# Optimization experiments

Measured on AMD Instinct MI355X. Metric: run time of the kernel, lower is better.

Reference implementation:

```python
import jax, jax.numpy as jnp
import numpy as np

N, P, C = 100000, 48, 8
D, H = 64, 4
DH = D // H
FLAG = 7
EPS = 1e-5


def _layer_norm(x, g, b):
    mu = x.mean(-1, keepdims=True)
    var = ((x - mu) ** 2).mean(-1, keepdims=True)
    return (x - mu) * jax.lax.rsqrt(var + EPS) * g + b


def setup_inputs() -> dict:
    key = jax.random.key(0)
    ks = jax.random.split(key, 24)
    w = lambda k, shp: (jax.random.normal(k, shp, dtype=jnp.float32) * 0.05)
    inp = {
        "voxel_features": jax.random.normal(ks[0], (N, D), dtype=jnp.float32),
        "voxels": jax.random.normal(ks[1], (N, P, C), dtype=jnp.float32),
        "pp_w1": w(ks[2], (D, C)), "pp_b1": w(ks[3], (D,)),
        "pp_w2": w(ks[4], (D, D)), "pp_b2": w(ks[5], (D,)),
        "in_proj_w": w(ks[6], (3 * D, D)), "in_proj_b": w(ks[7], (3 * D,)),
        "out_w": w(ks[8], (D, D)), "out_b": w(ks[9], (D,)),
        "ln1_g": jnp.ones((D,), jnp.float32), "ln1_b": jnp.zeros((D,), jnp.float32),
        "ffn_w1": w(ks[10], (2 * D, D)), "ffn_b1": w(ks[11], (2 * D,)),
        "ffn_w2": w(ks[12], (D, 2 * D)), "ffn_b2": w(ks[13], (D,)),
        "ln2_g": jnp.ones((D,), jnp.float32), "ln2_b": jnp.zeros((D,), jnp.float32),
        "op_w1": w(ks[14], (D, D)), "op_b1": w(ks[15], (D,)),
        "op_w2": w(ks[16], (D, D)), "op_b2": w(ks[17], (D,)),
        "num_points": jax.random.randint(ks[18], (N,), 0, P, dtype=jnp.int32),
    }
    return inp


def reference(voxel_features, voxels, pp_w1, pp_b1, pp_w2, pp_b2,
              in_proj_w, in_proj_b, out_w, out_b, ln1_g, ln1_b,
              ffn_w1, ffn_b1, ffn_w2, ffn_b2, ln2_g, ln2_b,
              op_w1, op_b1, op_w2, op_b2, num_points):
    n, p, _ = voxels.shape
    point_mask = jnp.arange(p)[None, :] < num_points[:, None]          # [N,P]
    current_mask = (voxels[:, :, FLAG] > 0.5) & point_mask             # [N,P]
    history_mask = point_mask & ~current_mask                          # [N,P]
    history_present = history_mask.any(axis=1, keepdims=True)          # [N,1]

    point_features = voxels[:, :, :C]

    def masked_mean(vals, mask):
        m = mask.astype(vals.dtype)[..., None]
        counts = jnp.clip(mask.sum(1, keepdims=True), 1, None).astype(vals.dtype)
        return (vals * m).sum(1) / counts                              # [N,C]

    cur_sum = masked_mean(point_features, current_mask)
    his_sum = masked_mean(point_features, history_mask)

    def point_proj(x):
        return jax.nn.relu(x @ pp_w1.T + pp_b1) @ pp_w2.T + pp_b2

    tokens = jnp.stack([voxel_features, point_proj(cur_sum), point_proj(his_sum)], axis=1)  # [N,3,D]

    key_pad = jnp.stack([jnp.zeros((n,), bool),
                         ~current_mask.any(1),
                         ~history_present[:, 0]], axis=1)              # [N,3]

    # multi-head self-attention over 3 tokens
    qkv = tokens @ in_proj_w.T + in_proj_b                             # [N,3,3D]
    q, k, v = jnp.split(qkv, 3, axis=-1)
    q = q.reshape(n, 3, H, DH).transpose(0, 2, 1, 3)                   # [N,H,3,DH]
    k = k.reshape(n, 3, H, DH).transpose(0, 2, 1, 3)
    v = v.reshape(n, 3, H, DH).transpose(0, 2, 1, 3)
    scores = jnp.einsum('nhqd,nhkd->nhqk', q, k) / np.sqrt(DH)
    scores = jnp.where(key_pad[:, None, None, :], -jnp.inf, scores)
    attn = jax.nn.softmax(scores, axis=-1)
    ctx = jnp.einsum('nhqk,nhkd->nhqd', attn, v)                       # [N,H,3,DH]
    ctx = ctx.transpose(0, 2, 1, 3).reshape(n, 3, D)
    attn_out = ctx @ out_w.T + out_b

    tokens = _layer_norm(tokens + attn_out, ln1_g, ln1_b)
    ffn = jax.nn.relu(tokens @ ffn_w1.T + ffn_b1) @ ffn_w2.T + ffn_b2
    tokens = _layer_norm(tokens + ffn, ln2_g, ln2_b)

    refined = jax.nn.relu(tokens[:, 0] @ op_w1.T + op_b1) @ op_w2.T + op_b2
    refined = refined * history_present.astype(refined.dtype)
    return voxel_features + refined
```

## Files before the change

kernel.cpp:

```cpp
#include <hip/hip_runtime.h>


using bf16x8 = __attribute__((ext_vector_type(8))) __bf16;
using f32x4  = __attribute__((ext_vector_type(4))) float;

#define DEV static __device__ __forceinline__
#define SYNC() __syncthreads()

DEV float bf2f(unsigned short u){
  union { unsigned int i; float f; } v; v.i = ((unsigned int)u) << 16; return v.f;
}
DEV unsigned short f2bf(float f){
  union { float f; unsigned int i; } v; v.f = f;
  unsigned int x = v.i;
  x += 0x7FFFu + ((x >> 16) & 1u);
  return (unsigned short)(x >> 16);
}

DEV unsigned short* lp(unsigned short* base, int row, int col){
  int byte = (col << 1) ^ ((row & 7) << 4);
  return (unsigned short*)((char*)base + (row << 7) + byte);
}

DEV bf16x8 ldA(const unsigned short* base, int mt, int kt, int lane){
  int row = mt*16 + (lane & 15);
  int col = kt*32 + ((lane >> 4) << 3);
  return *(const bf16x8*)lp((unsigned short*)base, row, col);
}
DEV bf16x8 ldB(const unsigned short* w, int frag, int lane){
  return *(const bf16x8*)(w + (size_t)frag*512 + (size_t)lane*8);
}
DEV void stC(unsigned short* base, int mt, int nt, f32x4 c, int lane){
  int col  = nt*16 + (lane & 15);
  int row0 = mt*16 + ((lane >> 4) << 2);
  #pragma unroll
  for (int r = 0; r < 4; ++r) *lp(base, row0 + r, col) = f2bf(c[r]);
}
DEV f32x4 MF(bf16x8 a, bf16x8 b, f32x4 c){
  return __builtin_amdgcn_mfma_f32_16x16x32_bf16(a, b, c, 0, 0, 0);
}

DEV void ld16(const unsigned short* base, int row, int col0, float* o){
  uint4 a = *(const uint4*)lp((unsigned short*)base, row, col0);
  uint4 b = *(const uint4*)lp((unsigned short*)base, row, col0 + 8);
  unsigned int w[8] = {a.x, a.y, a.z, a.w, b.x, b.y, b.z, b.w};
  #pragma unroll
  for (int i = 0; i < 8; ++i){
    union { unsigned int u; float f; } lo, hi;
    lo.u = w[i] << 16; hi.u = w[i] & 0xFFFF0000u;
    o[2*i] = lo.f; o[2*i+1] = hi.f;
  }
}
DEV void st16(unsigned short* base, int row, int col0, const float* f){
  unsigned int w[8];
  #pragma unroll
  for (int i = 0; i < 8; ++i)
    w[i] = (unsigned int)f2bf(f[2*i]) | ((unsigned int)f2bf(f[2*i+1]) << 16);
  *(uint4*)lp(base, row, col0)     = make_uint4(w[0], w[1], w[2], w[3]);
  *(uint4*)lp(base, row, col0 + 8) = make_uint4(w[4], w[5], w[6], w[7]);
}

DEV void layer_norm16(f32x4 x[4], const float* g, const float* b, int lane){
  float s[4], s2[4];
  #pragma unroll
  for (int r = 0; r < 4; ++r){
    s[r]  = x[0][r] + x[1][r] + x[2][r] + x[3][r];
    s2[r] = x[0][r]*x[0][r] + x[1][r]*x[1][r] + x[2][r]*x[2][r] + x[3][r]*x[3][r];
  }
  #pragma unroll
  for (int o = 1; o <= 8; o <<= 1){
    #pragma unroll
    for (int r = 0; r < 4; ++r){
      s[r]  += __shfl_xor(s[r],  o);
      s2[r] += __shfl_xor(s2[r], o);
    }
  }
  float mu[4], rs[4];
  #pragma unroll
  for (int r = 0; r < 4; ++r){
    mu[r] = s[r] * (1.f/64.f);
    float var = s2[r] * (1.f/64.f) - mu[r]*mu[r];
    rs[r] = rsqrtf(var + 1e-5f);
  }
  const int cl = lane & 15;
  #pragma unroll
  for (int nt = 0; nt < 4; ++nt){
    float gg = g[nt*16 + cl], bb = b[nt*16 + cl];
    #pragma unroll
    for (int r = 0; r < 4; ++r)
      x[nt][r] = (x[nt][r] - mu[r]) * rs[r] * gg + bb;
  }
}

__global__ void tva_pack_weights(const float* __restrict__ pp_w1, const float* __restrict__ pp_w2,
                                 const float* __restrict__ in_proj_w, const float* __restrict__ out_w,
                                 const float* __restrict__ ffn_w1, const float* __restrict__ ffn_w2,
                                 const float* __restrict__ op_w1, const float* __restrict__ op_w2,
                                 unsigned short* __restrict__ ws)
{
  int b = blockIdx.x, lane = threadIdx.x;
  const float* W; int base, ktiles, K;
  if      (b < 4)  { W = pp_w1;     base = 0;  ktiles = 1; K = 8;   }
  else if (b < 12) { W = pp_w2;     base = 4;  ktiles = 2; K = 64;  }
  else if (b < 36) { W = in_proj_w; base = 12; ktiles = 2; K = 64;  }
  else if (b < 44) { W = out_w;     base = 36; ktiles = 2; K = 64;  }
  else if (b < 60) { W = ffn_w1;    base = 44; ktiles = 2; K = 64;  }
  else if (b < 76) { W = ffn_w2;    base = 60; ktiles = 4; K = 128; }
  else if (b < 84) { W = op_w1;     base = 76; ktiles = 2; K = 64;  }
  else             { W = op_w2;     base = 84; ktiles = 2; K = 64;  }
  int local = b - base;
  int nt = local / ktiles, kt = local % ktiles;
  int n  = nt*16 + (lane & 15);
  int k0 = kt*32 + ((lane >> 4) << 3);
  unsigned short* dst = ws + (size_t)b*512 + (size_t)lane*8;
  #pragma unroll
  for (int i = 0; i < 8; ++i){
    int k = k0 + i;
    float v = (k < K) ? W[(size_t)n*K + k] : 0.0f;
    dst[i] = f2bf(v);
  }
}

__global__ __launch_bounds__(64, 2)
void tva_main(const float* __restrict__ vf, const float* __restrict__ vox,
              const int* __restrict__ num_points,
              const float* __restrict__ pp_b1, const float* __restrict__ pp_b2,
              const float* __restrict__ ipb,  const float* __restrict__ outb,
              const float* __restrict__ ln1g, const float* __restrict__ ln1b,
              const float* __restrict__ f1b,  const float* __restrict__ f2bv,
              const float* __restrict__ ln2g, const float* __restrict__ ln2b,
              const float* __restrict__ o1b,  const float* __restrict__ o2b,
              const unsigned short* __restrict__ wfrag,
              float* __restrict__ out)
{
  __shared__ unsigned short smem[(48 + 48 + 48 + 16) * 64];
  unsigned short* TOK = smem;
  unsigned short* KB  = smem + 48*64;
  unsigned short* VB  = smem + 96*64;
  unsigned short* SB  = smem + 144*64;

  const int lane = threadIdx.x;
  const int v0   = blockIdx.x * 16;
  const int cl   = lane & 15;

  const int vi = lane >> 2, pq = lane & 3;
  const int np = num_points[v0 + vi];
  float cs[8] = {0,0,0,0,0,0,0,0}, hs[8] = {0,0,0,0,0,0,0,0};
  float cc = 0.f, hc = 0.f;
  const float4* vp = (const float4*)(vox + (size_t)(v0 + vi) * 384);
  #pragma unroll
  for (int k = 0; k < 12; ++k){
    int p = pq + (k << 2);
    float4 a = vp[p*2], b = vp[p*2 + 1];
    float pm = (p < np) ? 1.f : 0.f;
    float cm = (b.w > 0.5f) ? pm : 0.f;
    float hm = pm - cm;
    cc += cm; hc += hm;
    cs[0] += a.x*cm; cs[1] += a.y*cm; cs[2] += a.z*cm; cs[3] += a.w*cm;
    cs[4] += b.x*cm; cs[5] += b.y*cm; cs[6] += b.z*cm; cs[7] += b.w*cm;
    hs[0] += a.x*hm; hs[1] += a.y*hm; hs[2] += a.z*hm; hs[3] += a.w*hm;
    hs[4] += b.x*hm; hs[5] += b.y*hm; hs[6] += b.z*hm; hs[7] += b.w*hm;
  }
  #pragma unroll
  for (int o = 1; o <= 2; o <<= 1){
    cc += __shfl_xor(cc, o); hc += __shfl_xor(hc, o);
    #pragma unroll
    for (int j = 0; j < 8; ++j){
      cs[j] += __shfl_xor(cs[j], o);
      hs[j] += __shfl_xor(hs[j], o);
    }
  }
  const float icc = 1.f / fmaxf(cc, 1.f);
  const float ihc = 1.f / fmaxf(hc, 1.f);
  const unsigned int myfw = (cc > 0.f ? 1u : 0u) | (hc > 0.f ? 2u : 0u);

  *lp(KB, vi,      pq*2)     = f2bf(cs[pq*2]   * icc);
  *lp(KB, vi,      pq*2 + 1) = f2bf(cs[pq*2+1] * icc);
  *lp(KB, 16 + vi, pq*2)     = f2bf(hs[pq*2]   * ihc);
  *lp(KB, 16 + vi, pq*2 + 1) = f2bf(hs[pq*2+1] * ihc);
  #pragma unroll
  for (int z = 0; z < 6; ++z){
    *lp(KB, vi,      8 + pq*6 + z) = 0;
    *lp(KB, 16 + vi, 8 + pq*6 + z) = 0;
  }
  SYNC();

  {
    bf16x8 ac  = ldA(KB, 0, 0, lane);
    bf16x8 ahs = ldA(KB, 1, 0, lane);
    #pragma unroll
    for (int nt = 0; nt < 4; ++nt){
      float bb = pp_b1[nt*16 + cl];
      f32x4 c0 = {bb, bb, bb, bb}, c1 = {bb, bb, bb, bb};
      bf16x8 B = ldB(wfrag, 0 + nt, lane);
      c0 = MF(ac,  B, c0);
      c1 = MF(ahs, B, c1);
      #pragma unroll
      for (int r = 0; r < 4; ++r){ c0[r] = fmaxf(c0[r], 0.f); c1[r] = fmaxf(c1[r], 0.f); }
      stC(VB, 0, nt, c0, lane);
      stC(VB, 1, nt, c1, lane);
    }
  }
  SYNC();
  {
    bf16x8 ah[2][2];
    #pragma unroll
    for (int m = 0; m < 2; ++m)
      #pragma unroll
      for (int kt = 0; kt < 2; ++kt) ah[m][kt] = ldA(VB, m, kt, lane);
    #pragma unroll
    for (int m = 0; m < 2; ++m){
      #pragma unroll
      for (int nt = 0; nt < 4; ++nt){
        float bb = pp_b2[nt*16 + cl];
        f32x4 c = {bb, bb, bb, bb};
        c = MF(ah[m][0], ldB(wfrag, 4 + nt*2 + 0, lane), c);
        c = MF(ah[m][1], ldB(wfrag, 4 + nt*2 + 1, lane), c);
        stC(TOK, m + 1, nt, c, lane);
      }
    }
  }
  {
    int rr = lane >> 2, q4 = lane & 3;
    const float* s = vf + (size_t)(v0 + rr)*64 + q4*16;
    float4 x0 = *(const float4*)(s +  0);
    float4 x1 = *(const float4*)(s +  4);
    float4 x2 = *(const float4*)(s +  8);
    float4 x3 = *(const float4*)(s + 12);
    float f[16] = {x0.x,x0.y,x0.z,x0.w, x1.x,x1.y,x1.z,x1.w,
                   x2.x,x2.y,x2.z,x2.w, x3.x,x3.y,x3.z,x3.w};
    st16(TOK, rr, q4*16, f);
  }
  SYNC();

  {
    bf16x8 at[3][2];
    #pragma unroll
    for (int m = 0; m < 3; ++m)
      #pragma unroll
      for (int kt = 0; kt < 2; ++kt) at[m][kt] = ldA(TOK, m, kt, lane);
    #pragma unroll
    for (int nt = 0; nt < 4; ++nt){
      float bb = ipb[nt*16 + cl];
      f32x4 c = {bb, bb, bb, bb};
      c = MF(at[0][0], ldB(wfrag, 12 + nt*2 + 0, lane), c);
      c = MF(at[0][1], ldB(wfrag, 12 + nt*2 + 1, lane), c);
      #pragma unroll
      for (int r = 0; r < 4; ++r) c[r] *= 0.25f;
      stC(SB, 0, nt, c, lane);
    }
    #pragma unroll
    for (int m = 0; m < 3; ++m){
      #pragma unroll
      for (int nt = 0; nt < 4; ++nt){
        int ntg = 4 + nt;
        float bb = ipb[64 + nt*16 + cl];
        f32x4 c = {bb, bb, bb, bb};
        c = MF(at[m][0], ldB(wfrag, 12 + ntg*2 + 0, lane), c);
        c = MF(at[m][1], ldB(wfrag, 12 + ntg*2 + 1, lane), c);
        stC(KB, m, nt, c, lane);
      }
    }
    #pragma unroll
    for (int m = 0; m < 3; ++m){
      #pragma unroll
      for (int nt = 0; nt < 4; ++nt){
        int ntg = 8 + nt;
        float bb = ipb[128 + nt*16 + cl];
        f32x4 c = {bb, bb, bb, bb};
        c = MF(at[m][0], ldB(wfrag, 12 + ntg*2 + 0, lane), c);
        c = MF(at[m][1], ldB(wfrag, 12 + ntg*2 + 1, lane), c);
        stC(VB, m, nt, c, lane);
      }
    }
  }
  SYNC();

  {
    const int av = lane & 15, hh = lane >> 4;
    unsigned int fw = (unsigned int)__shfl((int)myfw, av*4);
    bool ca = (fw & 1u) != 0, hp = (fw & 2u) != 0;
    float q[16]; ld16(SB, av, hh*16, q);
    float sc0, sc1, sc2;
    {
      float kv[16]; float d;
      ld16(KB, av,      hh*16, kv); d = 0.f;
      #pragma unroll
      for (int j = 0; j < 16; ++j) d += q[j]*kv[j];
      sc0 = d;
      ld16(KB, 16 + av, hh*16, kv); d = 0.f;
      #pragma unroll
      for (int j = 0; j < 16; ++j) d += q[j]*kv[j];
      sc1 = d;
      ld16(KB, 32 + av, hh*16, kv); d = 0.f;
      #pragma unroll
      for (int j = 0; j < 16; ++j) d += q[j]*kv[j];
      sc2 = d;
    }
    float m = sc0;
    m = ca ? fmaxf(m, sc1) : m;
    m = hp ? fmaxf(m, sc2) : m;
    float p0 = __expf(sc0 - m);
    float p1 = ca ? __expf(sc1 - m) : 0.f;
    float p2 = hp ? __expf(sc2 - m) : 0.f;
    float inv = 1.f / (p0 + p1 + p2);
    p0 *= inv; p1 *= inv; p2 *= inv;
    float ctx[16];
    {
      float vv[16];
      ld16(VB, av,      hh*16, vv);
      #pragma unroll
      for (int j = 0; j < 16; ++j) ctx[j] = p0*vv[j];
      ld16(VB, 16 + av, hh*16, vv);
      #pragma unroll
      for (int j = 0; j < 16; ++j) ctx[j] += p1*vv[j];
      ld16(VB, 32 + av, hh*16, vv);
      #pragma unroll
      for (int j = 0; j < 16; ++j) ctx[j] += p2*vv[j];
    }
    SYNC();
    st16(SB, av, hh*16, ctx);
  }
  SYNC();

  f32x4 res1[4];
  {
    bf16x8 a0 = ldA(SB, 0, 0, lane), a1 = ldA(SB, 0, 1, lane);
    const int r0 = (lane >> 4) << 2;
    #pragma unroll
    for (int nt = 0; nt < 4; ++nt){
      float bb = outb[nt*16 + cl];
      f32x4 c = {bb, bb, bb, bb};
      c = MF(a0, ldB(wfrag, 36 + nt*2 + 0, lane), c);
      c = MF(a1, ldB(wfrag, 36 + nt*2 + 1, lane), c);
      #pragma unroll
      for (int r = 0; r < 4; ++r)
        c[r] += bf2f(*lp(TOK, r0 + r, nt*16 + cl));
      res1[nt] = c;
    }
    layer_norm16(res1, ln1g, ln1b, lane);
    SYNC();
    #pragma unroll
    for (int nt = 0; nt < 4; ++nt) stC(TOK, 0, nt, res1[nt], lane);
  }
  SYNC();

  f32x4 tk2[4];
  {
    bf16x8 a0 = ldA(TOK, 0, 0, lane), a1 = ldA(TOK, 0, 1, lane);
    #pragma unroll
    for (int nt = 0; nt < 4; ++nt){
      float bb = f2bv[nt*16 + cl];
      tk2[nt] = (f32x4){bb, bb, bb, bb};
    }
    #pragma unroll
    for (int nt = 0; nt < 4; ++nt){
      float bb = f1b[nt*16 + cl];
      f32x4 c = {bb, bb, bb, bb};
      c = MF(a0, ldB(wfrag, 44 + nt*2 + 0, lane), c);
      c = MF(a1, ldB(wfrag, 44 + nt*2 + 1, lane), c);
      #pragma unroll
      for (int r = 0; r < 4; ++r) c[r] = fmaxf(c[r], 0.f);
      stC(SB, 0, nt, c, lane);
    }
    SYNC();
    {
      bf16x8 h0 = ldA(SB, 0, 0, lane), h1 = ldA(SB, 0, 1, lane);
      #pragma unroll
      for (int nt = 0; nt < 4; ++nt){
        tk2[nt] = MF(h0, ldB(wfrag, 60 + nt*4 + 0, lane), tk2[nt]);
        tk2[nt] = MF(h1, ldB(wfrag, 60 + nt*4 + 1, lane), tk2[nt]);
      }
    }
    SYNC();
    #pragma unroll
    for (int nt = 4; nt < 8; ++nt){
      float bb = f1b[nt*16 + cl];
      f32x4 c = {bb, bb, bb, bb};
      c = MF(a0, ldB(wfrag, 44 + nt*2 + 0, lane), c);
      c = MF(a1, ldB(wfrag, 44 + nt*2 + 1, lane), c);
      #pragma unroll
      for (int r = 0; r < 4; ++r) c[r] = fmaxf(c[r], 0.f);
      stC(SB, 0, nt - 4, c, lane);
    }
    SYNC();
    {
      bf16x8 h0 = ldA(SB, 0, 0, lane), h1 = ldA(SB, 0, 1, lane);
      #pragma unroll
      for (int nt = 0; nt < 4; ++nt){
        tk2[nt] = MF(h0, ldB(wfrag, 60 + nt*4 + 2, lane), tk2[nt]);
        tk2[nt] = MF(h1, ldB(wfrag, 60 + nt*4 + 3, lane), tk2[nt]);
      }
    }
    #pragma unroll
    for (int nt = 0; nt < 4; ++nt)
      #pragma unroll
      for (int r = 0; r < 4; ++r) tk2[nt][r] += res1[nt][r];
    layer_norm16(tk2, ln2g, ln2b, lane);
    SYNC();
    #pragma unroll
    for (int nt = 0; nt < 4; ++nt) stC(SB, 0, nt, tk2[nt], lane);
  }
  SYNC();

  {
    bf16x8 a0 = ldA(SB, 0, 0, lane), a1 = ldA(SB, 0, 1, lane);
    #pragma unroll
    for (int nt = 0; nt < 4; ++nt){
      float bb = o1b[nt*16 + cl];
      f32x4 c = {bb, bb, bb, bb};
      c = MF(a0, ldB(wfrag, 76 + nt*2 + 0, lane), c);
      c = MF(a1, ldB(wfrag, 76 + nt*2 + 1, lane), c);
      #pragma unroll
      for (int r = 0; r < 4; ++r) c[r] = fmaxf(c[r], 0.f);
      stC(KB, 0, nt, c, lane);
    }
    SYNC();
    bf16x8 b0 = ldA(KB, 0, 0, lane), b1 = ldA(KB, 0, 1, lane);
    const int r0 = (lane >> 4) << 2;
    #pragma unroll
    for (int nt = 0; nt < 4; ++nt){
      float bb = o2b[nt*16 + cl];
      f32x4 c = {bb, bb, bb, bb};
      c = MF(b0, ldB(wfrag, 84 + nt*2 + 0, lane), c);
      c = MF(b1, ldB(wfrag, 84 + nt*2 + 1, lane), c);
      #pragma unroll
      for (int r = 0; r < 4; ++r){
        int row = r0 + r;
        unsigned int fw2 = (unsigned int)__shfl((int)myfw, row*4);
        float keep = (fw2 & 2u) ? 1.f : 0.f;
        size_t idx = (size_t)(v0 + row)*64 + nt*16 + cl;
        out[idx] = vf[idx] + keep * c[r];
      }
    }
  }
}

extern "C" void kernel_launch(void* const* d_in, const int* in_sizes, int n_in,
                              void* d_out, int out_size, void* d_ws, size_t ws_size,
                              hipStream_t stream)
{
  (void)n_in; (void)out_size; (void)ws_size;
  const float* vf    = (const float*)d_in[0];
  const float* vox   = (const float*)d_in[1];
  const float* pp_w1 = (const float*)d_in[2];
  const float* pp_b1 = (const float*)d_in[3];
  const float* pp_w2 = (const float*)d_in[4];
  const float* pp_b2 = (const float*)d_in[5];
  const float* ipw   = (const float*)d_in[6];
  const float* ipb   = (const float*)d_in[7];
  const float* outw  = (const float*)d_in[8];
  const float* outb  = (const float*)d_in[9];
  const float* ln1g  = (const float*)d_in[10];
  const float* ln1b  = (const float*)d_in[11];
  const float* f1w   = (const float*)d_in[12];
  const float* f1b   = (const float*)d_in[13];
  const float* f2w   = (const float*)d_in[14];
  const float* f2b   = (const float*)d_in[15];
  const float* ln2g  = (const float*)d_in[16];
  const float* ln2b  = (const float*)d_in[17];
  const float* o1w   = (const float*)d_in[18];
  const float* o1b   = (const float*)d_in[19];
  const float* o2w   = (const float*)d_in[20];
  const float* o2b   = (const float*)d_in[21];
  const int*   npts  = (const int*)d_in[22];
  unsigned short* wfrag = (unsigned short*)d_ws;
  float* out = (float*)d_out;

  const int nvox = in_sizes[0] / 64;

  tva_pack_weights<<<92, 64, 0, stream>>>(pp_w1, pp_w2, ipw, outw, f1w, f2w, o1w, o2w, wfrag);
  tva_main<<<nvox / 16, 64, 0, stream>>>(vf, vox, npts, pp_b1, pp_b2, ipb, outb,
                                         ln1g, ln1b, f1b, f2b, ln2g, ln2b, o1b, o2b,
                                         wfrag, out);
}
```

Measured before the change: 77.27 us.

## Replace block barriers with per-wave LDS fences and pack two waves per block

Each wave now owns a private 64x64 LDS region, so __syncthreads is replaced by s_waitcnt lgkmcnt(0) fences. Blocks grow to two independent waves with launch bounds of 5 blocks. LDS use shrinks by computing V after attention scores and reusing buffers. Pre-MLP mean features are built in registers via shuffles, and voxel_features are loaded straight into MFMA fragments and kept in registers for the residual and output. This relies on intra-wave LDS ordering being sufficient, and ngrp/2 drops a trailing group if the group count is odd.

Result: slower. 118.0 us (+52.7%).

```diff
diff --git a/kernel.cpp b/kernel.cpp
--- a/kernel.cpp
+++ b/kernel.cpp
@@ -5,7 +5,7 @@
 using f32x4  = __attribute__((ext_vector_type(4))) float;
 
 #define DEV static __device__ __forceinline__
-#define SYNC() __syncthreads()
+#define FENCE() asm volatile("s_waitcnt lgkmcnt(0)" ::: "memory")
 
 DEV float bf2f(unsigned short u){
   union { unsigned int i; float f; } v; v.i = ((unsigned int)u) << 16; return v.f;
@@ -58,6 +58,13 @@
     w[i] = (unsigned int)f2bf(f[2*i]) | ((unsigned int)f2bf(f[2*i+1]) << 16);
   *(uint4*)lp(base, row, col0)     = make_uint4(w[0], w[1], w[2], w[3]);
   *(uint4*)lp(base, row, col0 + 8) = make_uint4(w[4], w[5], w[6], w[7]);
+}
+
+DEV bf16x8 pack8(const float* f){
+  union { bf16x8 v; unsigned short u[8]; } r;
+  #pragma unroll
+  for (int i = 0; i < 8; ++i) r.u[i] = f2bf(f[i]);
+  return r.v;
 }
 
 DEV void layer_norm16(f32x4 x[4], const float* g, const float* b, int lane){
@@ -121,7 +128,7 @@
   }
 }
 
-__global__ __launch_bounds__(64, 2)
+__global__ __launch_bounds__(128, 5)
 void tva_main(const float* __restrict__ vf, const float* __restrict__ vox,
               const int* __restrict__ num_points,
               const float* __restrict__ pp_b1, const float* __restrict__ pp_b2,
@@ -133,15 +140,15 @@
               const unsigned short* __restrict__ wfrag,
               float* __restrict__ out)
 {
-  __shared__ unsigned short smem[(48 + 48 + 48 + 16) * 64];
-  unsigned short* TOK = smem;
-  unsigned short* KB  = smem + 48*64;
-  unsigned short* VB  = smem + 96*64;
-  unsigned short* SB  = smem + 144*64;
-
-  const int lane = threadIdx.x;
-  const int v0   = blockIdx.x * 16;
-  const int cl   = lane & 15;
+  __shared__ unsigned short smem[2 * 64 * 64];
+  const int tid  = threadIdx.x;
+  const int wv   = tid >> 6;
+  const int lane = tid & 63;
+  unsigned short* X = smem + wv * (64*64);
+  unsigned short* Q = X + 48*64;
+  const int v0 = (blockIdx.x * 2 + wv) * 16;
+  const int cl = lane & 15;
+  const int r0 = (lane >> 4) << 2;
 
   const int vi = lane >> 2, pq = lane & 3;
   const int np = num_points[v0 + vi];
@@ -174,159 +181,165 @@
   const float ihc = 1.f / fmaxf(hc, 1.f);
   const unsigned int myfw = (cc > 0.f ? 1u : 0u) | (hc > 0.f ? 2u : 0u);
 
-  *lp(KB, vi,      pq*2)     = f2bf(cs[pq*2]   * icc);
-  *lp(KB, vi,      pq*2 + 1) = f2bf(cs[pq*2+1] * icc);
-  *lp(KB, 16 + vi, pq*2)     = f2bf(hs[pq*2]   * ihc);
-  *lp(KB, 16 + vi, pq*2 + 1) = f2bf(hs[pq*2+1] * ihc);
-  #pragma unroll
-  for (int z = 0; z < 6; ++z){
-    *lp(KB, vi,      8 + pq*6 + z) = 0;
-    *lp(KB, 16 + vi, 8 + pq*6 + z) = 0;
-  }
-  SYNC();
-
-  {
-    bf16x8 ac  = ldA(KB, 0, 0, lane);
-    bf16x8 ahs = ldA(KB, 1, 0, lane);
-    #pragma unroll
-    for (int nt = 0; nt < 4; ++nt){
-      float bb = pp_b1[nt*16 + cl];
-      f32x4 c0 = {bb, bb, bb, bb}, c1 = {bb, bb, bb, bb};
-      bf16x8 B = ldB(wfrag, 0 + nt, lane);
-      c0 = MF(ac,  B, c0);
-      c1 = MF(ahs, B, c1);
-      #pragma unroll
-      for (int r = 0; r < 4; ++r){ c0[r] = fmaxf(c0[r], 0.f); c1[r] = fmaxf(c1[r], 0.f); }
-      stC(VB, 0, nt, c0, lane);
-      stC(VB, 1, nt, c1, lane);
-    }
-  }
-  SYNC();
-  {
-    bf16x8 ah[2][2];
+  bf16x8 ac, ah;
+  {
+    const int src = cl * 4;
+    float cf[8], hf[8];
+    #pragma unroll
+    for (int i = 0; i < 8; ++i){
+      cf[i] = __shfl(cs[i]*icc, src);
+      hf[i] = __shfl(hs[i]*ihc, src);
+    }
+    union { bf16x8 v; unsigned short u[8]; } rc, rh;
+    #pragma unroll
+    for (int i = 0; i < 8; ++i){
+      rc.u[i] = (lane < 16) ? f2bf(cf[i]) : (unsigned short)0;
+      rh.u[i] = (lane < 16) ? f2bf(hf[i]) : (unsigned short)0;
+    }
+    ac = rc.v; ah = rh.v;
+  }
+
+  #pragma unroll
+  for (int nt = 0; nt < 4; ++nt){
+    float bb = pp_b1[nt*16 + cl];
+    f32x4 c0 = {bb, bb, bb, bb}, c1 = {bb, bb, bb, bb};
+    bf16x8 B = ldB(wfrag, nt, lane);
+    c0 = MF(ac, B, c0);
+    c1 = MF(ah, B, c1);
+    #pragma unroll
+    for (int r = 0; r < 4; ++r){ c0[r] = fmaxf(c0[r], 0.f); c1[r] = fmaxf(c1[r], 0.f); }
+    stC(X, 0, nt, c0, lane);
+    stC(X, 1, nt, c1, lane);
+  }
+  FENCE();
+  {
+    bf16x8 hfr[2][2];
     #pragma unroll
     for (int m = 0; m < 2; ++m)
       #pragma unroll
-      for (int kt = 0; kt < 2; ++kt) ah[m][kt] = ldA(VB, m, kt, lane);
+      for (int kt = 0; kt < 2; ++kt) hfr[m][kt] = ldA(X, m, kt, lane);
+    FENCE();
     #pragma unroll
     for (int m = 0; m < 2; ++m){
       #pragma unroll
       for (int nt = 0; nt < 4; ++nt){
         float bb = pp_b2[nt*16 + cl];
         f32x4 c = {bb, bb, bb, bb};
-        c = MF(ah[m][0], ldB(wfrag, 4 + nt*2 + 0, lane), c);
-        c = MF(ah[m][1], ldB(wfrag, 4 + nt*2 + 1, lane), c);
-        stC(TOK, m + 1, nt, c, lane);
+        c = MF(hfr[m][0], ldB(wfrag, 4 + nt*2 + 0, lane), c);
+        c = MF(hfr[m][1], ldB(wfrag, 4 + nt*2 + 1, lane), c);
+        stC(X, m, nt, c, lane);
       }
     }
   }
-  {
-    int rr = lane >> 2, q4 = lane & 3;
-    const float* s = vf + (size_t)(v0 + rr)*64 + q4*16;
-    float4 x0 = *(const float4*)(s +  0);
-    float4 x1 = *(const float4*)(s +  4);
-    float4 x2 = *(const float4*)(s +  8);
-    float4 x3 = *(const float4*)(s + 12);
-    float f[16] = {x0.x,x0.y,x0.z,x0.w, x1.x,x1.y,x1.z,x1.w,
-                   x2.x,x2.y,x2.z,x2.w, x3.x,x3.y,x3.z,x3.w};
-    st16(TOK, rr, q4*16, f);
-  }
-  SYNC();
-
-  {
-    bf16x8 at[3][2];
-    #pragma unroll
-    for (int m = 0; m < 3; ++m)
-      #pragma unroll
-      for (int kt = 0; kt < 2; ++kt) at[m][kt] = ldA(TOK, m, kt, lane);
-    #pragma unroll
-    for (int nt = 0; nt < 4; ++nt){
-      float bb = ipb[nt*16 + cl];
-      f32x4 c = {bb, bb, bb, bb};
-      c = MF(at[0][0], ldB(wfrag, 12 + nt*2 + 0, lane), c);
-      c = MF(at[0][1], ldB(wfrag, 12 + nt*2 + 1, lane), c);
-      #pragma unroll
-      for (int r = 0; r < 4; ++r) c[r] *= 0.25f;
-      stC(SB, 0, nt, c, lane);
-    }
+  FENCE();
+
+  bf16x8 at[3][2];
+  {
+    const float* s = vf + (size_t)(v0 + cl) * 64 + ((lane >> 4) << 3);
+    #pragma unroll
+    for (int kt = 0; kt < 2; ++kt){
+      float4 x0 = *(const float4*)(s + kt*32);
+      float4 x1 = *(const float4*)(s + kt*32 + 4);
+      float f[8] = {x0.x, x0.y, x0.z, x0.w, x1.x, x1.y, x1.z, x1.w};
+      at[0][kt] = pack8(f);
+    }
+    #pragma unroll
+    for (int kt = 0; kt < 2; ++kt){
+      at[1][kt] = ldA(X, 0, kt, lane);
+      at[2][kt] = ldA(X, 1, kt, lane);
+    }
+  }
+  FENCE();
+  #pragma unroll
+  for (int nt = 0; nt < 4; ++nt){
+    float bb = ipb[nt*16 + cl];
+    f32x4 c = {bb, bb, bb, bb};
+    c = MF(at[0][0], ldB(wfrag, 12 + nt*2 + 0, lane), c);
+    c = MF(at[0][1], ldB(wfrag, 12 + nt*2 + 1, lane), c);
+    #pragma unroll
+    for (int r = 0; r < 4; ++r) c[r] *= 0.25f;
+    stC(Q, 0, nt, c, lane);
+  }
+  #pragma unroll
+  for (int m = 0; m < 3; ++m){
+    #pragma unroll
+    for (int nt = 0; nt < 4; ++nt){
+      int ntg = 4 + nt;
+      float bb = ipb[64 + nt*16 + cl];
+      f32x4 c = {bb, bb, bb, bb};
+      c = MF(at[m][0], ldB(wfrag, 12 + ntg*2 + 0, lane), c);
+      c = MF(at[m][1], ldB(wfrag, 12 + ntg*2 + 1, lane), c);
+      stC(X, m, nt, c, lane);
+    }
+  }
+  FENCE();
+
+  const int av = cl, hh2 = lane >> 4;
+  float p0, p1, p2;
+  {
+    unsigned int fw = (unsigned int)__shfl((int)myfw, av*4);
+    bool caZ = (fw & 1u) != 0, hpZ = (fw & 2u) != 0;
+    float q[16]; ld16(Q, av, hh2*16, q);
+    float sc[3];
     #pragma unroll
     for (int m = 0; m < 3; ++m){
-      #pragma unroll
-      for (int nt = 0; nt < 4; ++nt){
-        int ntg = 4 + nt;
-        float bb = ipb[64 + nt*16 + cl];
-        f32x4 c = {bb, bb, bb, bb};
-        c = MF(at[m][0], ldB(wfrag, 12 + ntg*2 + 0, lane), c);
-        c = MF(at[m][1], ldB(wfrag, 12 + ntg*2 + 1, lane), c);
-        stC(KB, m, nt, c, lane);
-      }
-    }
-    #pragma unroll
-    for (int m = 0; m < 3; ++m){
-      #pragma unroll
-      for (int nt = 0; nt < 4; ++nt){
-        int ntg = 8 + nt;
-        float bb = ipb[128 + nt*16 + cl];
-        f32x4 c = {bb, bb, bb, bb};
-        c = MF(at[m][0], ldB(wfrag, 12 + ntg*2 + 0, lane), c);
-        c = MF(at[m][1], ldB(wfrag, 12 + ntg*2 + 1, lane), c);
-        stC(VB, m, nt, c, lane);
-      }
-    }
-  }
-  SYNC();
-
-  {
-    const int av = lane & 15, hh = lane >> 4;
-    unsigned int fw = (unsigned int)__shfl((int)myfw, av*4);
-    bool ca = (fw & 1u) != 0, hp = (fw & 2u) != 0;
-    float q[16]; ld16(SB, av, hh*16, q);
-    float sc0, sc1, sc2;
-    {
-      float kv[16]; float d;
-      ld16(KB, av,      hh*16, kv); d = 0.f;
+      float kv[16]; ld16(X, m*16 + av, hh2*16, kv);
+      float d = 0.f;
       #pragma unroll
       for (int j = 0; j < 16; ++j) d += q[j]*kv[j];
-      sc0 = d;
-      ld16(KB, 16 + av, hh*16, kv); d = 0.f;
-      #pragma unroll
-      for (int j = 0; j < 16; ++j) d += q[j]*kv[j];
-      sc1 = d;
-      ld16(KB, 32 + av, hh*16, kv); d = 0.f;
-      #pragma unroll
-      for (int j = 0; j < 16; ++j) d += q[j]*kv[j];
-      sc2 = d;
-    }
-    float m = sc0;
-    m = ca ? fmaxf(m, sc1) : m;
-    m = hp ? fmaxf(m, sc2) : m;
-    float p0 = __expf(sc0 - m);
-    float p1 = ca ? __expf(sc1 - m) : 0.f;
-    float p2 = hp ? __expf(sc2 - m) : 0.f;
+      sc[m] = d;
+    }
+    float mx = sc[0];
+    mx = caZ ? fmaxf(mx, sc[1]) : mx;
+    mx = hpZ ? fmaxf(mx, sc[2]) : mx;
+    p0 = __expf(sc[0] - mx);
+    p1 = caZ ? __expf(sc[1] - mx) : 0.f;
+    p2 = hpZ ? __expf(sc[2] - mx) : 0.f;
     float inv = 1.f / (p0 + p1 + p2);
     p0 *= inv; p1 *= inv; p2 *= inv;
+  }
+  FENCE();
+
+  #pragma unroll
+  for (int m = 0; m < 3; ++m){
+    #pragma unroll
+    for (int nt = 0; nt < 4; ++nt){
+      int ntg = 8 + nt;
+      float bb = ipb[128 + nt*16 + cl];
+      f32x4 c = {bb, bb, bb, bb};
+      c = MF(at[m][0], ldB(wfrag, 12 + ntg*2 + 0, lane), c);
+      c = MF(at[m][1], ldB(wfrag, 12 + ntg*2 + 1, lane), c);
+      stC(X, m, nt, c, lane);
+    }
+  }
+  FENCE();
+
+  {
     float ctx[16];
-    {
-      float vv[16];
-      ld16(VB, av,      hh*16, vv);
-      #pragma unroll
-      for (int j = 0; j < 16; ++j) ctx[j] = p0*vv[j];
-      ld16(VB, 16 + av, hh*16, vv);
-      #pragma unroll
-      for (int j = 0; j < 16; ++j) ctx[j] += p1*vv[j];
-      ld16(VB, 32 + av, hh*16, vv);
-      #pragma unroll
-      for (int j = 0; j < 16; ++j) ctx[j] += p2*vv[j];
-    }
-    SYNC();
-    st16(SB, av, hh*16, ctx);
-  }
-  SYNC();
+    float vv[16];
+    ld16(X, av, hh2*16, vv);
+    #pragma unroll
+    for (int j = 0; j < 16; ++j) ctx[j] = p0*vv[j];
+    ld16(X, 16 + av, hh2*16, vv);
+    #pragma unroll
+    for (int j = 0; j < 16; ++j) ctx[j] += p1*vv[j];
+    ld16(X, 32 + av, hh2*16, vv);
+    #pragma unroll
+    for (int j = 0; j < 16; ++j) ctx[j] += p2*vv[j];
+    st16(Q, av, hh2*16, ctx);
+  }
+  FENCE();
 
   f32x4 res1[4];
-  {
-    bf16x8 a0 = ldA(SB, 0, 0, lane), a1 = ldA(SB, 0, 1, lane);
-    const int r0 = (lane >> 4) << 2;
+  float resv[16];
+  {
+    bf16x8 a0 = ldA(Q, 0, 0, lane), a1 = ldA(Q, 0, 1, lane);
+    FENCE();
+    #pragma unroll
+    for (int nt = 0; nt < 4; ++nt)
+      #pragma unroll
+      for (int r = 0; r < 4; ++r)
+        resv[nt*4 + r] = vf[(size_t)(v0 + r0 + r)*64 + nt*16 + cl];
     #pragma unroll
     for (int nt = 0; nt < 4; ++nt){
       float bb = outb[nt*16 + cl];
@@ -334,20 +347,19 @@
       c = MF(a0, ldB(wfrag, 36 + nt*2 + 0, lane), c);
       c = MF(a1, ldB(wfrag, 36 + nt*2 + 1, lane), c);
       #pragma unroll
-      for (int r = 0; r < 4; ++r)
-        c[r] += bf2f(*lp(TOK, r0 + r, nt*16 + cl));
+      for (int r = 0; r < 4; ++r) c[r] += resv[nt*4 + r];
       res1[nt] = c;
     }
     layer_norm16(res1, ln1g, ln1b, lane);
-    SYNC();
-    #pragma unroll
-    for (int nt = 0; nt < 4; ++nt) stC(TOK, 0, nt, res1[nt], lane);
-  }
-  SYNC();
+    #pragma unroll
+    for (int nt = 0; nt < 4; ++nt) stC(Q, 0, nt, res1[nt], lane);
+  }
+  FENCE();
 
   f32x4 tk2[4];
   {
-    bf16x8 a0 = ldA(TOK, 0, 0, lane), a1 = ldA(TOK, 0, 1, lane);
+    bf16x8 a0 = ldA(Q, 0, 0, lane), a1 = ldA(Q, 0, 1, lane);
+    FENCE();
     #pragma unroll
     for (int nt = 0; nt < 4; ++nt){
       float bb = f2bv[nt*16 + cl];
@@ -361,18 +373,18 @@
       c = MF(a1, ldB(wfrag, 44 + nt*2 + 1, lane), c);
       #pragma unroll
       for (int r = 0; r < 4; ++r) c[r] = fmaxf(c[r], 0.f);
-      stC(SB, 0, nt, c, lane);
-    }
-    SYNC();
+      stC(X, 0, nt, c, lane);
+    }
+    FENCE();
     {
-      bf16x8 h0 = ldA(SB, 0, 0, lane), h1 = ldA(SB, 0, 1, lane);
+      bf16x8 h0 = ldA(X, 0, 0, lane), h1 = ldA(X, 0, 1, lane);
+      FENCE();
       #pragma unroll
       for (int nt = 0; nt < 4; ++nt){
         tk2[nt] = MF(h0, ldB(wfrag, 60 + nt*4 + 0, lane), tk2[nt]);
         tk2[nt] = MF(h1, ldB(wfrag, 60 + nt*4 + 1, lane), tk2[nt]);
       }
     }
-    SYNC();
     #pragma unroll
     for (int nt = 4; nt < 8; ++nt){
       float bb = f1b[nt*16 + cl];
@@ -381,11 +393,12 @@
       c = MF(a1, ldB(wfrag, 44 + nt*2 + 1, lane), c);
       #pragma unroll
       for (int r = 0; r < 4; ++r) c[r] = fmaxf(c[r], 0.f);
-      stC(SB, 0, nt - 4, c, lane);
-    }
-    SYNC();
+      stC(X, 0, nt - 4, c, lane);
+    }
+    FENCE();
     {
-      bf16x8 h0 = ldA(SB, 0, 0, lane), h1 = ldA(SB, 0, 1, lane);
+      bf16x8 h0 = ldA(X, 0, 0, lane), h1 = ldA(X, 0, 1, lane);
+      FENCE();
       #pragma unroll
       for (int nt = 0; nt < 4; ++nt){
         tk2[nt] = MF(h0, ldB(wfrag, 60 + nt*4 + 2, lane), tk2[nt]);
@@ -397,14 +410,14 @@
       #pragma unroll
       for (int r = 0; r < 4; ++r) tk2[nt][r] += res1[nt][r];
     layer_norm16(tk2, ln2g, ln2b, lane);
-    SYNC();
-    #pragma unroll
-    for (int nt = 0; nt < 4; ++nt) stC(SB, 0, nt, tk2[nt], lane);
-  }
-  SYNC();
-
-  {
-    bf16x8 a0 = ldA(SB, 0, 0, lane), a1 = ldA(SB, 0, 1, lane);
+    #pragma unroll
+    for (int nt = 0; nt < 4; ++nt) stC(Q, 0, nt, tk2[nt], lane);
+  }
+  FENCE();
+
+  {
+    bf16x8 a0 = ldA(Q, 0, 0, lane), a1 = ldA(Q, 0, 1, lane);
+    FENCE();
     #pragma unroll
     for (int nt = 0; nt < 4; ++nt){
       float bb = o1b[nt*16 + cl];
@@ -413,11 +426,11 @@
       c = MF(a1, ldB(wfrag, 76 + nt*2 + 1, lane), c);
       #pragma unroll
       for (int r = 0; r < 4; ++r) c[r] = fmaxf(c[r], 0.f);
-      stC(KB, 0, nt, c, lane);
-    }
-    SYNC();
-    bf16x8 b0 = ldA(KB, 0, 0, lane), b1 = ldA(KB, 0, 1, lane);
-    const int r0 = (lane >> 4) << 2;
+      stC(X, 0, nt, c, lane);
+    }
+    FENCE();
+    bf16x8 b0 = ldA(X, 0, 0, lane), b1 = ldA(X, 0, 1, lane);
+    FENCE();
     #pragma unroll
     for (int nt = 0; nt < 4; ++nt){
       float bb = o2b[nt*16 + cl];
@@ -430,7 +443,7 @@
         unsigned int fw2 = (unsigned int)__shfl((int)myfw, row*4);
         float keep = (fw2 & 2u) ? 1.f : 0.f;
         size_t idx = (size_t)(v0 + row)*64 + nt*16 + cl;
-        out[idx] = vf[idx] + keep * c[r];
+        out[idx] = resv[nt*4 + r] + keep * c[r];
       }
     }
   }
@@ -468,9 +481,9 @@
   float* out = (float*)d_out;
 
   const int nvox = in_sizes[0] / 64;
-
+  const int ngrp = nvox / 16;
   tva_pack_weights<<<92, 64, 0, stream>>>(pp_w1, pp_w2, ipw, outw, f1w, f2w, o1w, o2w, wfrag);
-  tva_main<<<nvox / 16, 64, 0, stream>>>(vf, vox, npts, pp_b1, pp_b2, ipb, outb,
+  tva_main<<<ngrp / 2, 128, 0, stream>>>(vf, vox, npts, pp_b1, pp_b2, ipb, outb,
                                          ln1g, ln1b, f1b, f2b, ln2g, ln2b, o1b, o2b,
                                          wfrag, out);
 }
```
